# Kernel tuning notes

Hardware: AMD Instinct MI355X
Metric: run time of the kernel (lower is better)

Reference implementation:

```python
import jax, jax.numpy as jnp
import numpy as np

BLOCK = 64
# NF4 codebook (normal-float 4-bit values, as in QLoRA/torchao)
NF4_TABLE = jnp.array([
    -1.0, -0.6961928009986877, -0.5250730514526367, -0.39491748809814453,
    -0.28444138169288635, -0.18477343022823334, -0.09105003625154495, 0.0,
    0.07958029955625534, 0.16093020141124725, 0.24611230194568634,
    0.33791524171829224, 0.44070982933044434, 0.5626170039176941,
    0.7229568362236023, 1.0], dtype=jnp.float32)

D_MODEL, HIDDEN = 4096, 11008
BATCH, SEQ = 2, 2048


def setup_inputs() -> dict:
    key = jax.random.key(0)
    ks = jax.random.split(key, 7)
    x = jax.random.normal(ks[0], (BATCH, SEQ, D_MODEL), dtype=jnp.float32)
    w1_q = jax.random.randint(ks[1], (HIDDEN, D_MODEL), 0, 16, dtype=jnp.int32)
    w2_q = jax.random.randint(ks[2], (HIDDEN, D_MODEL), 0, 16, dtype=jnp.int32)
    w3_q = jax.random.randint(ks[3], (D_MODEL, HIDDEN), 0, 16, dtype=jnp.int32)
    # per-block absmax scales (positive, typical weight magnitude ~0.02)
    w1_scale = jax.random.uniform(ks[4], (HIDDEN, D_MODEL // BLOCK), dtype=jnp.float32) * 0.04
    w2_scale = jax.random.uniform(ks[5], (HIDDEN, D_MODEL // BLOCK), dtype=jnp.float32) * 0.04
    w3_scale = jax.random.uniform(ks[6], (D_MODEL, HIDDEN // BLOCK), dtype=jnp.float32) * 0.04
    return {"x": x, "w1_q": w1_q, "w1_scale": w1_scale,
            "w2_q": w2_q, "w2_scale": w2_scale,
            "w3_q": w3_q, "w3_scale": w3_scale}


def dequant_nf4(q, scale):
    # q: [O, I] int codes in [0,16); scale: [O, I//BLOCK]
    O, I = q.shape
    vals = NF4_TABLE[q]                               # lookup -> [O, I]
    vals = vals.reshape(O, I // BLOCK, BLOCK) * scale[:, :, None]
    return vals.reshape(O, I)


def reference(x, w1_q, w1_scale, w2_q, w2_scale, w3_q, w3_scale):
    w1 = dequant_nf4(w1_q, w1_scale)                  # [H, D]
    w2 = dequant_nf4(w2_q, w2_scale)                  # [H, D]
    w3 = dequant_nf4(w3_q, w3_scale)                  # [D, H]
    h = jax.nn.silu(jnp.einsum('bsd,hd->bsh', x, w1)) * jnp.einsum('bsd,hd->bsh', x, w2)
    return jnp.einsum('bsh,dh->bsd', h, w3)
```

## Files before the change

### kernel.cpp

```cpp
#include <hip/hip_runtime.h>
#include <hip/hip_bf16.h>

typedef unsigned short u16;
typedef __bf16  bf16x8 __attribute__((ext_vector_type(8)));
typedef float   f32x4  __attribute__((ext_vector_type(4)));

__device__ __constant__ float NF4C[16] = {
    -1.0f, -0.6961928009986877f, -0.5250730514526367f, -0.39491748809814453f,
    -0.28444138169288635f, -0.18477343022823334f, -0.09105003625154495f, 0.0f,
    0.07958029955625534f, 0.16093020141124725f, 0.24611230194568634f,
    0.33791524171829224f, 0.44070982933044434f, 0.5626170039176941f,
    0.7229568362236023f, 1.0f };

__device__ __forceinline__ u16 f2bf(float f) {
    union { float f; unsigned u; } v; v.f = f;
    unsigned r = v.u + 0x7FFFu + ((v.u >> 16) & 1u);
    return (u16)(r >> 16);
}
__device__ __forceinline__ float bf2f(u16 b) {
    union { unsigned u; float f; } v; v.u = ((unsigned)b) << 16;
    return v.f;
}

__device__ __forceinline__ void gl2lds16(const void* g, void* l) {
    __builtin_amdgcn_global_load_lds(
        (__attribute__((address_space(1))) void*)g,
        (__attribute__((address_space(3))) void*)l,
        16, 0, 0);
}

#define WAITVM(N) asm volatile("s_waitcnt vmcnt(" #N ")" ::: "memory")

__global__ __launch_bounds__(256) void cast_f32_bf16(
    const float* __restrict__ in, u16* __restrict__ out, int n8) {
    int i = blockIdx.x * 256 + threadIdx.x;
    if (i >= n8) return;
    const float4* p = (const float4*)in + (size_t)i * 2;
    float4 a = p[0], b = p[1];
    union { u16 u[8]; uint4 v; } r;
    r.u[0] = f2bf(a.x); r.u[1] = f2bf(a.y); r.u[2] = f2bf(a.z); r.u[3] = f2bf(a.w);
    r.u[4] = f2bf(b.x); r.u[5] = f2bf(b.y); r.u[6] = f2bf(b.z); r.u[7] = f2bf(b.w);
    ((uint4*)out)[i] = r.v;
}

__global__ __launch_bounds__(256) void dequant_nf4(
    const int* __restrict__ q, const float* __restrict__ s,
    u16* __restrict__ w, int I, int spr) {
    __shared__ float tab[16];
    if (threadIdx.x < 16) tab[threadIdx.x] = NF4C[threadIdx.x];
    __syncthreads();
    int col = (blockIdx.x * 256 + threadIdx.x) * 8;
    if (col >= I) return;
    int row = blockIdx.y;
    size_t base = (size_t)row * I + col;
    int4 c0 = *(const int4*)(q + base);
    int4 c1 = *(const int4*)(q + base + 4);
    float sc = s[(size_t)row * spr + (col >> 6)];
    union { u16 u[8]; uint4 v; } r;
    r.u[0] = f2bf(tab[c0.x & 15] * sc);
    r.u[1] = f2bf(tab[c0.y & 15] * sc);
    r.u[2] = f2bf(tab[c0.z & 15] * sc);
    r.u[3] = f2bf(tab[c0.w & 15] * sc);
    r.u[4] = f2bf(tab[c1.x & 15] * sc);
    r.u[5] = f2bf(tab[c1.y & 15] * sc);
    r.u[6] = f2bf(tab[c1.z & 15] * sc);
    r.u[7] = f2bf(tab[c1.w & 15] * sc);
    *(uint4*)(w + base) = r.v;
}

template<int EPI>
__global__ __launch_bounds__(512, 2) void gemm_bt(
    const u16* __restrict__ A, const u16* __restrict__ B,
    void* Cout, const u16* gate, int K, int ldc) {
    __shared__ u16 lA[2 * 16384];
    __shared__ u16 lB[2 * 16384];

    const int tid  = threadIdx.x;
    const int lane = tid & 63;
    const int wv   = tid >> 6;

    const int NT = gridDim.x, MT = gridDim.y;
    int id  = blockIdx.y * NT + blockIdx.x;
    int nid = (id & 7) * ((NT * MT) >> 3) + (id >> 3);
    const int bx = nid / MT;
    const int by = nid - bx * MT;

    const int sr = lane >> 2;
    const int sq = (lane & 3) ^ ((sr >> 1) & 3);

    const int gA0 = ((wv & 4) << 1) + (wv & 3);
    const int gA1 = gA0 + 4;
    const int gB0 = ((wv >> 1) << 2) + (wv & 1);
    const int gB1 = gB0 + 2;

    const u16* pA0 = A + (size_t)(by * 256 + gA0 * 16 + sr) * K + (sq << 3);
    const u16* pA1 = A + (size_t)(by * 256 + gA1 * 16 + sr) * K + (sq << 3);
    const u16* pB0 = B + (size_t)(bx * 256 + gB0 * 16 + sr) * K + (sq << 3);
    const u16* pB1 = B + (size_t)(bx * 256 + gB1 * 16 + sr) * K + (sq << 3);

    const int sA0 = gA0 * 512 + lane * 8;
    const int sA1 = gA1 * 512 + lane * 8;
    const int sB0 = gB0 * 512 + lane * 8;
    const int sB1 = gB1 * 512 + lane * 8;

    const int r16    = lane & 15;
    const int pq     = lane >> 4;
    const int slot16 = (r16 << 2) + (pq ^ ((r16 >> 1) & 3));
    const int aBase  = ((wv & 1) << 12) + slot16 * 8;
    const int bBase  = ((wv >> 1) << 11) + slot16 * 8;

#define STG_A0(TT, D) do { const u16* g_ = pA0 + (size_t)(TT) * 64;       \
        u16* l_ = lA + ((D) << 14) + sA0;                                 \
        gl2lds16(g_, l_); gl2lds16(g_ + 32, l_ + 8192); } while (0)
#define STG_A1(TT, D) do { const u16* g_ = pA1 + (size_t)(TT) * 64;       \
        u16* l_ = lA + ((D) << 14) + sA1;                                 \
        gl2lds16(g_, l_); gl2lds16(g_ + 32, l_ + 8192); } while (0)
#define STG_B0(TT, D) do { const u16* g_ = pB0 + (size_t)(TT) * 64;       \
        u16* l_ = lB + ((D) << 14) + sB0;                                 \
        gl2lds16(g_, l_); gl2lds16(g_ + 32, l_ + 8192); } while (0)
#define STG_B1(TT, D) do { const u16* g_ = pB1 + (size_t)(TT) * 64;       \
        u16* l_ = lB + ((D) << 14) + sB1;                                 \
        gl2lds16(g_, l_); gl2lds16(g_ + 32, l_ + 8192); } while (0)

#define DSR_A(C_, QM) do {                                                \
        const u16* b_ = lA + ((C_) << 14) + aBase + (QM) * 4 * 512;       \
        _Pragma("unroll")                                                 \
        for (int mm = 0; mm < 4; ++mm) {                                  \
            af[mm * 2 + 0] = *(const bf16x8*)(b_ + mm * 512);             \
            af[mm * 2 + 1] = *(const bf16x8*)(b_ + mm * 512 + 8192);      \
        } } while (0)
#define DSR_B(C_, QN) do {                                                \
        const u16* b_ = lB + ((C_) << 14) + bBase + (QN) * 2 * 512;       \
        _Pragma("unroll")                                                 \
        for (int jj = 0; jj < 2; ++jj) {                                  \
            bf[(QN) * 4 + jj * 2 + 0] = *(const bf16x8*)(b_ + jj * 512);  \
            bf[(QN) * 4 + jj * 2 + 1] = *(const bf16x8*)(b_ + jj * 512 + 8192); \
        } } while (0)

#define MFMA_Q(QM, QN) do {                                               \
        _Pragma("unroll")                                                 \
        for (int mm = 0; mm < 4; ++mm)                                    \
        _Pragma("unroll")                                                 \
        for (int jj = 0; jj < 2; ++jj) {                                  \
            f32x4 c_ = acc[(QM) * 4 + mm][(QN) * 2 + jj];                 \
            c_ = __builtin_amdgcn_mfma_f32_16x16x32_bf16(                 \
                af[mm * 2 + 0], bf[(QN) * 4 + jj * 2 + 0], c_, 0, 0, 0);  \
            c_ = __builtin_amdgcn_mfma_f32_16x16x32_bf16(                 \
                af[mm * 2 + 1], bf[(QN) * 4 + jj * 2 + 1], c_, 0, 0, 0);  \
            acc[(QM) * 4 + mm][(QN) * 2 + jj] = c_;                       \
        } } while (0)

#define PH_OPEN() do {                                                    \
        __builtin_amdgcn_sched_barrier(0);                                \
        __builtin_amdgcn_s_barrier();                                     \
        asm volatile("s_waitcnt lgkmcnt(0)" ::: "memory");                \
        __builtin_amdgcn_sched_barrier(0);                                \
        __builtin_amdgcn_s_setprio(1); } while (0)
#define PH_CLOSE() do {                                                   \
        __builtin_amdgcn_s_setprio(0);                                    \
        __builtin_amdgcn_sched_barrier(0);                                \
        __builtin_amdgcn_s_barrier();                                     \
        __builtin_amdgcn_sched_barrier(0); } while (0)
#define PH_CLOSE_VM() do {                                                \
        __builtin_amdgcn_s_setprio(0);                                    \
        __builtin_amdgcn_sched_barrier(0);                                \
        WAITVM(4);                                                        \
        __builtin_amdgcn_s_barrier();                                     \
        __builtin_amdgcn_sched_barrier(0); } while (0)

    f32x4 acc[8][4] = {};
    bf16x8 af[8], bf[8];
    const int KT = K >> 6;

    STG_A0(0, 0); STG_B0(0, 0); STG_A1(0, 0); STG_B1(0, 0);
    STG_A0(1, 1); STG_B0(1, 1);
    WAITVM(4);
    __builtin_amdgcn_s_barrier();
    __builtin_amdgcn_sched_barrier(0);

    for (int T = 0; T < KT; ++T) {
        const int c  = T & 1, o = c ^ 1;
        const int t1 = (T + 1 < KT) ? T + 1 : KT - 1;
        const int t2 = (T + 2 < KT) ? T + 2 : KT - 1;
        DSR_A(c, 0); DSR_B(c, 0);
        STG_A1(t1, o);
        PH_OPEN(); MFMA_Q(0, 0); PH_CLOSE();
        DSR_B(c, 1);
        STG_B1(t1, o);
        PH_OPEN(); MFMA_Q(0, 1); PH_CLOSE();
        DSR_A(c, 1);
        STG_A0(t2, c);
        PH_OPEN(); MFMA_Q(1, 0); PH_CLOSE();
        STG_B0(t2, c);
        PH_OPEN(); MFMA_Q(1, 1); PH_CLOSE_VM();
    }

    const int en   = lane & 15;
    const int er   = (lane >> 4) << 2;
    const int row0 = by * 256 + ((wv & 1) << 7);
    const int col0 = bx * 256 + ((wv >> 1) << 6);
    #pragma unroll
    for (int i = 0; i < 8; ++i) {
        int rowb = row0 + i * 16 + er;
        #pragma unroll
        for (int j = 0; j < 4; ++j) {
            int col = col0 + j * 16 + en;
            #pragma unroll
            for (int r = 0; r < 4; ++r) {
                size_t idx = (size_t)(rowb + r) * ldc + col;
                float v = acc[i][j][r];
                if (EPI == 0) {
                    ((u16*)Cout)[idx] = f2bf(v);
                } else if (EPI == 1) {
                    float g = bf2f(gate[idx]);
                    float sg = g / (1.0f + __expf(-g));
                    ((u16*)Cout)[idx] = f2bf(sg * v);
                } else {
                    ((float*)Cout)[idx] = v;
                }
            }
        }
    }
#undef STG_A0
#undef STG_A1
#undef STG_B0
#undef STG_B1
#undef DSR_A
#undef DSR_B
#undef MFMA_Q
#undef PH_OPEN
#undef PH_CLOSE
#undef PH_CLOSE_VM
}

extern "C" void kernel_launch(void* const* d_in, const int* in_sizes, int n_in,
                              void* d_out, int out_size, void* d_ws, size_t ws_size,
                              hipStream_t stream) {
    const float* x   = (const float*)d_in[0];
    const int*   w1q = (const int*)d_in[1];
    const float* w1s = (const float*)d_in[2];
    const int*   w2q = (const int*)d_in[3];
    const float* w2s = (const float*)d_in[4];
    const int*   w3q = (const int*)d_in[5];
    const float* w3s = (const float*)d_in[6];
    float* out = (float*)d_out;

    const int M = 4096, D = 4096, H = 11008;

    u16* xb = (u16*)d_ws;
    u16* wb = xb + (size_t)M * D;
    u16* hb = wb + (size_t)H * D;

    cast_f32_bf16<<<(M * D / 8 + 255) / 256, 256, 0, stream>>>(x, xb, M * D / 8);

    dim3 dqg1((D / 8 + 255) / 256, H);
    dequant_nf4<<<dqg1, 256, 0, stream>>>(w1q, w1s, wb, D, D / 64);
    gemm_bt<0><<<dim3(H / 256, M / 256), 512, 0, stream>>>(xb, wb, hb, nullptr, D, H);

    dequant_nf4<<<dqg1, 256, 0, stream>>>(w2q, w2s, wb, D, D / 64);
    gemm_bt<1><<<dim3(H / 256, M / 256), 512, 0, stream>>>(xb, wb, hb, hb, D, H);

    dim3 dqg3((H / 8 + 255) / 256, D);
    dequant_nf4<<<dqg3, 256, 0, stream>>>(w3q, w3s, wb, H, H / 64);
    gemm_bt<2><<<dim3(D / 256, M / 256), 512, 0, stream>>>(hb, wb, out, nullptr, H, D);
}
```

Baseline: 1.794 ms.

## Double-buffer LDS fragment registers to overlap ds_reads with MFMA phases

Splits the A/B register fragments into two sets so the next quadrant's LDS reads are issued before the current MFMA block, and prefetches the next K-tile's first fragments at the end of each iteration. It removes the per-phase lgkmcnt(0) waits and halves the barriers per phase, tightens the vmcnt wait, and relies on the compiler's automatic waits. The aim is to hide LDS read latency behind matrix ops. In exchange it uses more VGPRs and adds risk of race or stall ordering issues with fewer barriers.

```diff
diff --git a/kernel.cpp b/kernel.cpp
--- a/kernel.cpp
+++ b/kernel.cpp
@@ -30,6 +30,8 @@
 }
 
 #define WAITVM(N) asm volatile("s_waitcnt vmcnt(" #N ")" ::: "memory")
+#define SCHED0()  __builtin_amdgcn_sched_barrier(0)
+#define BAR()     __builtin_amdgcn_s_barrier()
 
 __global__ __launch_bounds__(256) void cast_f32_bf16(
     const float* __restrict__ in, u16* __restrict__ out, int n8) {
@@ -122,77 +124,66 @@
         u16* l_ = lB + ((D) << 14) + sB1;                                 \
         gl2lds16(g_, l_); gl2lds16(g_ + 32, l_ + 8192); } while (0)
 
-#define DSR_A(C_, QM) do {                                                \
-        const u16* b_ = lA + ((C_) << 14) + aBase + (QM) * 4 * 512;       \
+#define DSR_AF(DST, C_, QM) do {                                          \
+        const u16* b_ = lA + ((C_) << 14) + aBase + (QM) * (4 * 512);     \
         _Pragma("unroll")                                                 \
         for (int mm = 0; mm < 4; ++mm) {                                  \
-            af[mm * 2 + 0] = *(const bf16x8*)(b_ + mm * 512);             \
-            af[mm * 2 + 1] = *(const bf16x8*)(b_ + mm * 512 + 8192);      \
+            DST[mm * 2 + 0] = *(const bf16x8*)(b_ + mm * 512);            \
+            DST[mm * 2 + 1] = *(const bf16x8*)(b_ + mm * 512 + 8192);     \
         } } while (0)
-#define DSR_B(C_, QN) do {                                                \
-        const u16* b_ = lB + ((C_) << 14) + bBase + (QN) * 2 * 512;       \
+#define DSR_BF(DST, C_, QN) do {                                          \
+        const u16* b_ = lB + ((C_) << 14) + bBase + (QN) * (2 * 512);     \
         _Pragma("unroll")                                                 \
         for (int jj = 0; jj < 2; ++jj) {                                  \
-            bf[(QN) * 4 + jj * 2 + 0] = *(const bf16x8*)(b_ + jj * 512);  \
-            bf[(QN) * 4 + jj * 2 + 1] = *(const bf16x8*)(b_ + jj * 512 + 8192); \
+            DST[jj * 2 + 0] = *(const bf16x8*)(b_ + jj * 512);            \
+            DST[jj * 2 + 1] = *(const bf16x8*)(b_ + jj * 512 + 8192);     \
         } } while (0)
 
-#define MFMA_Q(QM, QN) do {                                               \
+#define MFMA_Q(QM, QN, AF, BF) do {                                       \
+        __builtin_amdgcn_s_setprio(1);                                    \
         _Pragma("unroll")                                                 \
         for (int mm = 0; mm < 4; ++mm)                                    \
         _Pragma("unroll")                                                 \
         for (int jj = 0; jj < 2; ++jj) {                                  \
             f32x4 c_ = acc[(QM) * 4 + mm][(QN) * 2 + jj];                 \
             c_ = __builtin_amdgcn_mfma_f32_16x16x32_bf16(                 \
-                af[mm * 2 + 0], bf[(QN) * 4 + jj * 2 + 0], c_, 0, 0, 0);  \
+                AF[mm * 2 + 0], BF[jj * 2 + 0], c_, 0, 0, 0);             \
             c_ = __builtin_amdgcn_mfma_f32_16x16x32_bf16(                 \
-                af[mm * 2 + 1], bf[(QN) * 4 + jj * 2 + 1], c_, 0, 0, 0);  \
+                AF[mm * 2 + 1], BF[jj * 2 + 1], c_, 0, 0, 0);             \
             acc[(QM) * 4 + mm][(QN) * 2 + jj] = c_;                       \
-        } } while (0)
-
-#define PH_OPEN() do {                                                    \
-        __builtin_amdgcn_sched_barrier(0);                                \
-        __builtin_amdgcn_s_barrier();                                     \
-        asm volatile("s_waitcnt lgkmcnt(0)" ::: "memory");                \
-        __builtin_amdgcn_sched_barrier(0);                                \
-        __builtin_amdgcn_s_setprio(1); } while (0)
-#define PH_CLOSE() do {                                                   \
-        __builtin_amdgcn_s_setprio(0);                                    \
-        __builtin_amdgcn_sched_barrier(0);                                \
-        __builtin_amdgcn_s_barrier();                                     \
-        __builtin_amdgcn_sched_barrier(0); } while (0)
-#define PH_CLOSE_VM() do {                                                \
-        __builtin_amdgcn_s_setprio(0);                                    \
-        __builtin_amdgcn_sched_barrier(0);                                \
-        WAITVM(4);                                                        \
-        __builtin_amdgcn_s_barrier();                                     \
-        __builtin_amdgcn_sched_barrier(0); } while (0)
+        }                                                                 \
+        __builtin_amdgcn_s_setprio(0); } while (0)
 
     f32x4 acc[8][4] = {};
-    bf16x8 af[8], bf[8];
+    bf16x8 afA[8], afB[8], bfA[4], bfB[4];
     const int KT = K >> 6;
 
     STG_A0(0, 0); STG_B0(0, 0); STG_A1(0, 0); STG_B1(0, 0);
     STG_A0(1, 1); STG_B0(1, 1);
     WAITVM(4);
-    __builtin_amdgcn_s_barrier();
-    __builtin_amdgcn_sched_barrier(0);
+    BAR(); SCHED0();
+    DSR_AF(afA, 0, 0); DSR_BF(bfA, 0, 0);
 
     for (int T = 0; T < KT; ++T) {
         const int c  = T & 1, o = c ^ 1;
         const int t1 = (T + 1 < KT) ? T + 1 : KT - 1;
         const int t2 = (T + 2 < KT) ? T + 2 : KT - 1;
-        DSR_A(c, 0); DSR_B(c, 0);
+        DSR_BF(bfB, c, 1);
         STG_A1(t1, o);
-        PH_OPEN(); MFMA_Q(0, 0); PH_CLOSE();
-        DSR_B(c, 1);
+        SCHED0(); BAR(); SCHED0();
+        MFMA_Q(0, 0, afA, bfA);
+        DSR_AF(afB, c, 1);
         STG_B1(t1, o);
-        PH_OPEN(); MFMA_Q(0, 1); PH_CLOSE();
-        DSR_A(c, 1);
+        SCHED0(); BAR(); SCHED0();
+        MFMA_Q(0, 1, afA, bfB);
         STG_A0(t2, c);
-        PH_OPEN(); MFMA_Q(1, 0); PH_CLOSE();
+        SCHED0(); BAR(); SCHED0();
+        MFMA_Q(1, 0, afB, bfA);
         STG_B0(t2, c);
-        PH_OPEN(); MFMA_Q(1, 1); PH_CLOSE_VM();
+        WAITVM(2);
+        SCHED0(); BAR(); SCHED0();
+        DSR_AF(afA, o, 0); DSR_BF(bfA, o, 0);
+        MFMA_Q(1, 1, afB, bfB);
     }
 
     const int en   = lane & 15;
@@ -225,12 +216,9 @@
 #undef STG_A1
 #undef STG_B0
 #undef STG_B1
-#undef DSR_A
-#undef DSR_B
+#undef DSR_AF
+#undef DSR_BF
 #undef MFMA_Q
-#undef PH_OPEN
-#undef PH_CLOSE
-#undef PH_CLOSE_VM
 }
 
 extern "C" void kernel_launch(void* const* d_in, const int* in_sizes, int n_in,
```

New measurement: 1.937 ms. +7.9%, slower.

## Merge GEMM k-loop into two phases per tile and unroll by two

Applied to the files above, without the earlier changes.

Restructures the 256x256 bf16 MFMA main loop from four barrier-delimited phases per K tile to two, issuing more LDS reads and global-to-LDS stages before each barrier. The loop is also unrolled by two so the double-buffer index is a compile-time constant. This aims to halve barrier and waitcnt overhead per tile and give longer MFMA bursts. In exchange it raises register pressure from holding more fragments at once, and it assumes KT is even, which holds for K=4096 and K=11008.

```diff
diff --git a/kernel.cpp b/kernel.cpp
--- a/kernel.cpp
+++ b/kernel.cpp
@@ -29,7 +29,10 @@
         16, 0, 0);
 }
 
-#define WAITVM(N) asm volatile("s_waitcnt vmcnt(" #N ")" ::: "memory")
+#define WAITVM(N)  asm volatile("s_waitcnt vmcnt(" #N ")" ::: "memory")
+#define WAITLG(N)  asm volatile("s_waitcnt lgkmcnt(" #N ")" ::: "memory")
+#define SCHED0()   __builtin_amdgcn_sched_barrier(0)
+#define BAR()      __builtin_amdgcn_s_barrier()
 
 __global__ __launch_bounds__(256) void cast_f32_bf16(
     const float* __restrict__ in, u16* __restrict__ out, int n8) {
@@ -123,14 +126,14 @@
         gl2lds16(g_, l_); gl2lds16(g_ + 32, l_ + 8192); } while (0)
 
 #define DSR_A(C_, QM) do {                                                \
-        const u16* b_ = lA + ((C_) << 14) + aBase + (QM) * 4 * 512;       \
+        const u16* b_ = lA + ((C_) << 14) + aBase + (QM) * (4 * 512);     \
         _Pragma("unroll")                                                 \
         for (int mm = 0; mm < 4; ++mm) {                                  \
             af[mm * 2 + 0] = *(const bf16x8*)(b_ + mm * 512);             \
             af[mm * 2 + 1] = *(const bf16x8*)(b_ + mm * 512 + 8192);      \
         } } while (0)
 #define DSR_B(C_, QN) do {                                                \
-        const u16* b_ = lB + ((C_) << 14) + bBase + (QN) * 2 * 512;       \
+        const u16* b_ = lB + ((C_) << 14) + bBase + (QN) * (2 * 512);     \
         _Pragma("unroll")                                                 \
         for (int jj = 0; jj < 2; ++jj) {                                  \
             bf[(QN) * 4 + jj * 2 + 0] = *(const bf16x8*)(b_ + jj * 512);  \
@@ -150,23 +153,32 @@
             acc[(QM) * 4 + mm][(QN) * 2 + jj] = c_;                       \
         } } while (0)
 
-#define PH_OPEN() do {                                                    \
-        __builtin_amdgcn_sched_barrier(0);                                \
-        __builtin_amdgcn_s_barrier();                                     \
-        asm volatile("s_waitcnt lgkmcnt(0)" ::: "memory");                \
-        __builtin_amdgcn_sched_barrier(0);                                \
-        __builtin_amdgcn_s_setprio(1); } while (0)
-#define PH_CLOSE() do {                                                   \
+#define KTILE(T_, C_, O_) do {                                            \
+        const int t1_ = ((T_) + 1 < KT) ? (T_) + 1 : KT - 1;              \
+        const int t2_ = ((T_) + 2 < KT) ? (T_) + 2 : KT - 1;              \
+                                          \
+        DSR_A(C_, 0); DSR_B(C_, 0); DSR_B(C_, 1);                         \
+        STG_A1(t1_, O_); STG_B1(t1_, O_);                                 \
+        WAITLG(8);                                                        \
+        SCHED0(); BAR();                                                  \
+        WAITLG(0);                                                        \
+        SCHED0();                                                         \
+        __builtin_amdgcn_s_setprio(1);                                    \
+        MFMA_Q(0, 0); MFMA_Q(0, 1);                                       \
         __builtin_amdgcn_s_setprio(0);                                    \
-        __builtin_amdgcn_sched_barrier(0);                                \
-        __builtin_amdgcn_s_barrier();                                     \
-        __builtin_amdgcn_sched_barrier(0); } while (0)
-#define PH_CLOSE_VM() do {                                                \
+        SCHED0(); BAR(); SCHED0();                                        \
+                                          \
+        DSR_A(C_, 1);                                                     \
+        STG_A0(t2_, C_); STG_B0(t2_, C_);                                 \
+        WAITVM(4);                                                        \
+        SCHED0(); BAR();                                                  \
+        WAITLG(0);                                                        \
+        SCHED0();                                                         \
+        __builtin_amdgcn_s_setprio(1);                                    \
+        MFMA_Q(1, 0); MFMA_Q(1, 1);                                       \
         __builtin_amdgcn_s_setprio(0);                                    \
-        __builtin_amdgcn_sched_barrier(0);                                \
-        WAITVM(4);                                                        \
-        __builtin_amdgcn_s_barrier();                                     \
-        __builtin_amdgcn_sched_barrier(0); } while (0)
+        SCHED0(); BAR(); SCHED0();                                        \
+    } while (0)
 
     f32x4 acc[8][4] = {};
     bf16x8 af[8], bf[8];
@@ -175,24 +187,11 @@
     STG_A0(0, 0); STG_B0(0, 0); STG_A1(0, 0); STG_B1(0, 0);
     STG_A0(1, 1); STG_B0(1, 1);
     WAITVM(4);
-    __builtin_amdgcn_s_barrier();
-    __builtin_amdgcn_sched_barrier(0);
-
-    for (int T = 0; T < KT; ++T) {
-        const int c  = T & 1, o = c ^ 1;
-        const int t1 = (T + 1 < KT) ? T + 1 : KT - 1;
-        const int t2 = (T + 2 < KT) ? T + 2 : KT - 1;
-        DSR_A(c, 0); DSR_B(c, 0);
-        STG_A1(t1, o);
-        PH_OPEN(); MFMA_Q(0, 0); PH_CLOSE();
-        DSR_B(c, 1);
-        STG_B1(t1, o);
-        PH_OPEN(); MFMA_Q(0, 1); PH_CLOSE();
-        DSR_A(c, 1);
-        STG_A0(t2, c);
-        PH_OPEN(); MFMA_Q(1, 0); PH_CLOSE();
-        STG_B0(t2, c);
-        PH_OPEN(); MFMA_Q(1, 1); PH_CLOSE_VM();
+    BAR(); SCHED0();
+
+    for (int T = 0; T < KT; T += 2) {
+        KTILE(T, 0, 1);
+        KTILE(T + 1, 1, 0);
     }
 
     const int en   = lane & 15;
@@ -228,9 +227,7 @@
 #undef DSR_A
 #undef DSR_B
 #undef MFMA_Q
-#undef PH_OPEN
-#undef PH_CLOSE
-#undef PH_CLOSE_VM
+#undef KTILE
 }
 
 extern "C" void kernel_launch(void* const* d_in, const int* in_sizes, int n_in,
```

After: 1.710 ms. 1.05x faster.
